# Kernel optimization log

Measured on AMD Instinct MI355X. Metric: run time of the kernel, lower is better.

The kernel has to match this reference:

```python
import jax, jax.numpy as jnp
import numpy as np

B, D, H, O, E, K = 8192, 1024, 4096, 1024, 8, 2

def setup_inputs() -> dict:
    key = jax.random.key(0)
    ks = jax.random.split(key, 8)
    x = jax.random.normal(ks[0], (B, D), dtype=jnp.float32)
    topk_idx = jax.random.randint(ks[1], (B, K), 0, E, dtype=jnp.int32)
    weights = jax.random.uniform(ks[2], (B, K), dtype=jnp.float32)
    s1 = 1.0 / np.sqrt(D)
    s2 = 1.0 / np.sqrt(H)
    W1 = jax.random.uniform(ks[3], (E, D, H), minval=-s1, maxval=s1, dtype=jnp.float32)
    b1 = jax.random.uniform(ks[4], (E, H), minval=-s1, maxval=s1, dtype=jnp.float32)
    W2 = jax.random.uniform(ks[5], (E, H, O), minval=-s2, maxval=s2, dtype=jnp.float32)
    b2 = jax.random.uniform(ks[6], (E, O), minval=-s2, maxval=s2, dtype=jnp.float32)
    return {"x": x, "topk_idx": topk_idx, "weights": weights,
            "W1": W1, "b1": b1, "W2": W2, "b2": b2}

def reference(x, topk_idx, weights, W1, b1, W2, b2):
    # Per-token gate mass for each expert: gate[b,e] = sum_i weights[b,i]*[topk_idx[b,i]==e]
    # Equivalent to the original masked gather/scatter combine (duplicates in topk_idx sum).
    out = jnp.zeros((x.shape[0], W2.shape[-1]), dtype=x.dtype)
    for e in range(W1.shape[0]):  # small fixed loop over experts
        gate_e = jnp.sum(weights * (topk_idx == e), axis=1)  # [B]
        h = jax.nn.relu(x @ W1[e] + b1[e])                   # [B,H]
        out_e = h @ W2[e] + b2[e]                            # [B,O]
        out = out + gate_e[:, None] * out_e
    return out
```

## Files before the change

### kernel.cpp

```cpp
#include <hip/hip_runtime.h>
#include <stdint.h>

#define B_TOK 8192
#define D_DIM 1024
#define H_DIM 4096
#define O_DIM 1024
#define E_NUM 8
#define K_TOP 2
#define NPAIR (B_TOK * K_TOP)

typedef short bf16x8 __attribute__((ext_vector_type(8)));
typedef float f32x4 __attribute__((ext_vector_type(4)));

struct Hdr {
    int counts[8];
    int offsets[9];
    int cursor[8];
    int total1, total2;
    int base1[9];
    int base2[9];
};

__device__ __forceinline__ unsigned short f2bf(float f) {
    union { float f; unsigned int u; } v; v.f = f;
    unsigned int u = v.u;
    unsigned int r = (u + 0x7fffu + ((u >> 16) & 1u)) >> 16;
    return (unsigned short)r;
}

__device__ __forceinline__ float bf2f(unsigned short s) {
    union { unsigned int u; float f; } v;
    v.u = ((unsigned int)s) << 16;
    return v.f;
}

__device__ __forceinline__ void async16(const void* g, const void* l) {
    __builtin_amdgcn_global_load_lds(
        (__attribute__((address_space(1))) void*)(uintptr_t)g,
        (__attribute__((address_space(3))) void*)(uint32_t)(uintptr_t)l,
        16, 0, 0);
}


__global__ void cvt_x_kernel(const float* __restrict__ x, unsigned short* __restrict__ xb) {
    int i = (blockIdx.x * 256 + threadIdx.x) * 4;
    float4 v = *(const float4*)(x + i);
    ushort4 o;
    o.x = f2bf(v.x); o.y = f2bf(v.y); o.z = f2bf(v.z); o.w = f2bf(v.w);
    *(ushort4*)(xb + i) = o;
}

__global__ __launch_bounds__(256) void tconv_kernel(const float* __restrict__ in,
                                                    unsigned short* __restrict__ out,
                                                    int R, int C) {
    __shared__ float t[64 * 69];
    int e = blockIdx.z;
    const float* ip = in + (size_t)e * R * C;
    unsigned short* op = out + (size_t)e * R * C;
    int c0 = blockIdx.x * 64, r0 = blockIdx.y * 64;
    int tid = threadIdx.x;
    int lr = tid >> 4;
    int lc = (tid & 15) * 4;
#pragma unroll
    for (int i = 0; i < 4; i++) {
        int row = lr + i * 16;
        float4 v = *(const float4*)&ip[(size_t)(r0 + row) * C + c0 + lc];
        t[row * 69 + lc + 0] = v.x;
        t[row * 69 + lc + 1] = v.y;
        t[row * 69 + lc + 2] = v.z;
        t[row * 69 + lc + 3] = v.w;
    }
    __syncthreads();
#pragma unroll
    for (int i = 0; i < 4; i++) {
        int c = lr + i * 16;
        ushort4 o;
        o.x = f2bf(t[(lc + 0) * 69 + c]);
        o.y = f2bf(t[(lc + 1) * 69 + c]);
        o.z = f2bf(t[(lc + 2) * 69 + c]);
        o.w = f2bf(t[(lc + 3) * 69 + c]);
        *(ushort4*)&op[(size_t)(c0 + c) * R + r0 + lc] = o;
    }
}


__global__ void route_count_kernel(const int* __restrict__ topk, Hdr* hdr) {
    __shared__ int cnt[8];
    int tid = threadIdx.x;
    if (tid < 8) cnt[tid] = 0;
    __syncthreads();
    for (int i = tid; i < NPAIR; i += 1024) atomicAdd(&cnt[topk[i]], 1);
    __syncthreads();
    if (tid == 0) {
        int off = 0, t1 = 0, t2 = 0;
        for (int e = 0; e < 8; e++) {
            int c = cnt[e];
            hdr->counts[e] = c;
            hdr->offsets[e] = off;
            hdr->cursor[e] = off;
            hdr->base1[e] = t1;
            hdr->base2[e] = t2;
            int mt = (c + 255) >> 8;
            t1 += mt * (H_DIM / 256);
            t2 += mt * (O_DIM / 256);
            off += c;
        }
        hdr->offsets[8] = off;
        hdr->base1[8] = t1;
        hdr->base2[8] = t2;
        hdr->total1 = t1;
        hdr->total2 = t2;
    }
}

__global__ void route_fill_kernel(const int* __restrict__ topk, const float* __restrict__ wts,
                                  Hdr* hdr, int* __restrict__ ptok, float* __restrict__ pgate,
                                  int* __restrict__ pslot) {
    int i = blockIdx.x * 256 + threadIdx.x;
    int e = topk[i];
    int pos = atomicAdd(&hdr->cursor[e], 1);
    ptok[pos] = i >> 1;
    pgate[pos] = wts[i];
    pslot[i] = pos;
}

__global__ void ws_fail_kernel(float* out) { out[0] = 1.0e9f; }


#define ASL(BUF, KH) ((BUF) * 32768 + (KH) * 16384)

#define STG_A(BUF, KH, KOFF) do { \
    async16(Ab + srcA[0] + (KOFF), smem + ASL(BUF, KH) + wu * 2048); \
    async16(Ab + srcA[1] + (KOFF), smem + ASL(BUF, KH) + wu * 2048 + 1024); } while (0)

#define STG_B(BUF, KH, KOFF) do { \
    async16(Bb + srcB[0] + (KOFF), smem + 65536 + ASL(BUF, KH) + wu * 2048); \
    async16(Bb + srcB[1] + (KOFF), smem + 65536 + ASL(BUF, KH) + wu * 2048 + 1024); } while (0)

#define VM6 asm volatile("s_waitcnt vmcnt(6)" ::: "memory")
#define VM0 asm volatile("s_waitcnt vmcnt(0)" ::: "memory")
#define NOPX ((void)0)

#define PHASE0(BUF, KH, STAGE, CKPT) do { \
    STAGE; \
    bq[0] = *(const bf16x8*)&smem[pBo[0] + ASL(BUF, KH)]; \
    bq[1] = *(const bf16x8*)&smem[pBo[1] + ASL(BUF, KH)]; \
    bq[2] = *(const bf16x8*)&smem[pBo[2] + ASL(BUF, KH)]; \
    bq[3] = *(const bf16x8*)&smem[pBo[3] + ASL(BUF, KH)]; \
    aq[0] = *(const bf16x8*)&smem[pAo[0] + ASL(BUF, KH)]; \
    aq[1] = *(const bf16x8*)&smem[pAo[1] + ASL(BUF, KH)]; \
    aq[2] = *(const bf16x8*)&smem[pAo[2] + ASL(BUF, KH)]; \
    aq[3] = *(const bf16x8*)&smem[pAo[3] + ASL(BUF, KH)]; \
    __builtin_amdgcn_s_barrier(); \
    asm volatile("s_waitcnt lgkmcnt(0)" ::: "memory"); \
    __builtin_amdgcn_s_setprio(1); \
    _Pragma("unroll") \
    for (int q_ = 0; q_ < 4; ++q_) { \
        _Pragma("unroll") \
        for (int n_ = 0; n_ < 4; ++n_) \
            acc[q_][n_] = __builtin_amdgcn_mfma_f32_16x16x32_bf16(aq[q_], bq[n_], acc[q_][n_], 0, 0, 0); \
    } \
    __builtin_amdgcn_s_setprio(0); \
    CKPT; \
    __builtin_amdgcn_s_barrier(); \
} while (0)

#define PHASE1(BUF, KH, STAGE, CKPT) do { \
    STAGE; \
    aq[0] = *(const bf16x8*)&smem[pAo[4] + ASL(BUF, KH)]; \
    aq[1] = *(const bf16x8*)&smem[pAo[5] + ASL(BUF, KH)]; \
    aq[2] = *(const bf16x8*)&smem[pAo[6] + ASL(BUF, KH)]; \
    aq[3] = *(const bf16x8*)&smem[pAo[7] + ASL(BUF, KH)]; \
    __builtin_amdgcn_s_barrier(); \
    asm volatile("s_waitcnt lgkmcnt(0)" ::: "memory"); \
    __builtin_amdgcn_s_setprio(1); \
    _Pragma("unroll") \
    for (int q_ = 0; q_ < 4; ++q_) { \
        _Pragma("unroll") \
        for (int n_ = 0; n_ < 4; ++n_) \
            acc[4 + q_][n_] = __builtin_amdgcn_mfma_f32_16x16x32_bf16(aq[q_], bq[n_], acc[4 + q_][n_], 0, 0, 0); \
    } \
    __builtin_amdgcn_s_setprio(0); \
    CKPT; \
    __builtin_amdgcn_s_barrier(); \
} while (0)

template <int KD, int N, bool GATHER>
__global__ __launch_bounds__(512, 2) void moe_gemm_kernel(
    const unsigned short* __restrict__ A,
    const unsigned short* __restrict__ Bt,
    const float* __restrict__ bias,
    const Hdr* __restrict__ hdr,
    const int* __restrict__ ptok,
    unsigned short* __restrict__ outp) {

    extern __shared__ __align__(16) char smem[];
    constexpr int NT = KD / 64;
    constexpr int NI = NT / 2;
    static_assert(NT >= 4 && (NT % 2) == 0, "K-tile count");

    const int tid = threadIdx.x;
    const int lane = tid & 63;
    const int wv = tid >> 6;
    const int wu = __builtin_amdgcn_readfirstlane(wv);
    const int lr = lane & 15;
    const int lkg = lane >> 4;
    const int wr = wv >> 2;
    const int wc = wv & 3;

    const int total = GATHER ? hdr->total1 : hdr->total2;
    const int* tb = GATHER ? hdr->base1 : hdr->base2;

    int chunk = (total + 7) >> 3;
    int seq = (blockIdx.x & 7) * chunk + (blockIdx.x >> 3);
    if (seq >= total) return;

    int e = 0;
#pragma unroll
    for (int j = 1; j < 8; j++)
        if (seq >= tb[j]) e = j;
    e = __builtin_amdgcn_readfirstlane(e);
    int lt = seq - tb[e];
    int cnt = hdr->counts[e], off = hdr->offsets[e];
    int MT = (cnt + 255) >> 8;
    int mtile = lt % MT, ntile = lt / MT;
    int m0 = mtile * 256, n0 = ntile * 256;

    const char* Ab = (const char*)A;
    const char* Bb = (const char*)(Bt + (size_t)e * ((size_t)N * KD));

    uint32_t srcA[2], srcB[2];
#pragma unroll
    for (int l = 0; l < 2; ++l) {
        int p = wv * 128 + l * 64 + lane;
        int rp = p >> 2, cp = p & 3;
        int r = rp ^ ((rp >> 2) & 1);
        int c = cp ^ (r & 3);
        int q = off + m0 + r;
        q = q > NPAIR - 1 ? NPAIR - 1 : q;
        uint32_t rowA = GATHER ? (uint32_t)ptok[q] : (uint32_t)q;
        srcA[l] = rowA * (uint32_t)(KD * 2) + (uint32_t)(c * 16);
        srcB[l] = (uint32_t)(n0 + r) * (uint32_t)(KD * 2) + (uint32_t)(c * 16);
    }

    uint32_t pAo[8], pBo[4];
#pragma unroll
    for (int mr = 0; mr < 8; ++mr) {
        int r = wr * 128 + mr * 16 + lr;
        pAo[mr] = (uint32_t)((r ^ ((r >> 2) & 1)) * 64 + (lkg ^ (r & 3)) * 16);
    }
#pragma unroll
    for (int nr = 0; nr < 4; ++nr) {
        int r = wc * 64 + nr * 16 + lr;
        pBo[nr] = (uint32_t)(65536 + (r ^ ((r >> 2) & 1)) * 64 + (lkg ^ (r & 3)) * 16);
    }

    f32x4 acc[8][4];
#pragma unroll
    for (int i = 0; i < 8; ++i)
#pragma unroll
        for (int j = 0; j < 4; ++j)
            acc[i][j] = (f32x4){0.f, 0.f, 0.f, 0.f};
    bf16x8 aq[4], bq[4];

    STG_A(0, 0, 0u);   STG_B(0, 0, 0u);
    STG_A(0, 1, 64u);  STG_B(0, 1, 64u);
    STG_A(1, 0, 128u); STG_B(1, 0, 128u);
    STG_B(1, 1, 192u);
    VM0;
    __builtin_amdgcn_s_barrier();

    for (int it = 0; it < NI - 1; ++it) {
        const uint32_t kb = (uint32_t)it * 256u;
        PHASE0(0, 0, STG_A(1, 1, kb + 192u), NOPX);
        PHASE1(0, 0, STG_B(0, 0, kb + 256u), NOPX);
        PHASE0(0, 1, STG_A(0, 0, kb + 256u), NOPX);
        PHASE1(0, 1, STG_B(0, 1, kb + 320u), VM6);
        PHASE0(1, 0, STG_A(0, 1, kb + 320u), NOPX);
        PHASE1(1, 0, STG_B(1, 0, kb + 384u), NOPX);
        PHASE0(1, 1, STG_A(1, 0, kb + 384u), NOPX);
        PHASE1(1, 1, STG_B(1, 1, kb + 448u), VM6);
    }
    {
        const uint32_t kb = (uint32_t)(NI - 1) * 256u;
        PHASE0(0, 0, STG_A(1, 1, kb + 192u), NOPX);
        PHASE1(0, 0, NOPX, NOPX);
        PHASE0(0, 1, NOPX, NOPX);
        PHASE1(0, 1, NOPX, VM0);
        PHASE0(1, 0, NOPX, NOPX);
        PHASE1(1, 0, NOPX, NOPX);
        PHASE0(1, 1, NOPX, NOPX);
        PHASE1(1, 1, NOPX, NOPX);
    }

    int rows_valid = cnt - m0;
    if (rows_valid > 256) rows_valid = 256;
#pragma unroll
    for (int nr = 0; nr < 4; ++nr) {
        int n = wc * 64 + nr * 16 + lr;
        float bv = bias[(size_t)e * N + n0 + n];
#pragma unroll
        for (int mr = 0; mr < 8; ++mr) {
#pragma unroll
            for (int r2 = 0; r2 < 4; ++r2) {
                int m = wr * 128 + mr * 16 + lkg * 4 + r2;
                float v = acc[mr][nr][r2] + bv;
                if (GATHER) v = v > 0.f ? v : 0.f;
                *(unsigned short*)&smem[(m * 256 + n) * 2] = f2bf(v);
            }
        }
    }
    __syncthreads();
#pragma unroll
    for (int j = 0; j < 16; ++j) {
        int idx = j * 512 + tid;
        int row = idx >> 5;
        int c16 = idx & 31;
        if (row < rows_valid) {
            uint4 v = *(const uint4*)&smem[row * 512 + c16 * 16];
            *(uint4*)&outp[(size_t)(off + m0 + row) * N + n0 + c16 * 8] = v;
        }
    }
}

__global__ void combine_kernel(const unsigned short* __restrict__ oslot,
                               const int* __restrict__ pslot,
                               const float* __restrict__ wts,
                               float* __restrict__ out) {
    int tok = blockIdx.x;
    int s0 = pslot[tok * 2], s1 = pslot[tok * 2 + 1];
    float g0 = wts[tok * 2], g1 = wts[tok * 2 + 1];
    int n = threadIdx.x * 4;
    ushort4 a = *(const ushort4*)&oslot[(size_t)s0 * O_DIM + n];
    ushort4 b = *(const ushort4*)&oslot[(size_t)s1 * O_DIM + n];
    float4 o;
    o.x = g0 * bf2f(a.x) + g1 * bf2f(b.x);
    o.y = g0 * bf2f(a.y) + g1 * bf2f(b.y);
    o.z = g0 * bf2f(a.z) + g1 * bf2f(b.z);
    o.w = g0 * bf2f(a.w) + g1 * bf2f(b.w);
    *(float4*)&out[(size_t)tok * O_DIM + n] = o;
}


extern "C" void kernel_launch(void* const* d_in, const int* in_sizes, int n_in,
                              void* d_out, int out_size, void* d_ws, size_t ws_size,
                              hipStream_t stream) {
    const float* x   = (const float*)d_in[0];
    const int* topk  = (const int*)d_in[1];
    const float* wts = (const float*)d_in[2];
    const float* W1  = (const float*)d_in[3];
    const float* b1  = (const float*)d_in[4];
    const float* W2  = (const float*)d_in[5];
    const float* b2  = (const float*)d_in[6];
    float* out = (float*)d_out;

    char* ws = (char*)d_ws;
    size_t off = 0;
    auto alloc = [&](size_t bytes) -> void* {
        void* p = ws + off;
        off += (bytes + 255) & ~(size_t)255;
        return p;
    };
    Hdr* hdr = (Hdr*)alloc(sizeof(Hdr));
    int* ptok = (int*)alloc((size_t)NPAIR * 4);
    float* pgate = (float*)alloc((size_t)NPAIR * 4);
    int* pslot = (int*)alloc((size_t)NPAIR * 4);
    unsigned short* xb   = (unsigned short*)alloc((size_t)B_TOK * D_DIM * 2);
    unsigned short* W1bt = (unsigned short*)alloc((size_t)E_NUM * D_DIM * H_DIM * 2);
    unsigned short* W2bt = (unsigned short*)alloc((size_t)E_NUM * H_DIM * O_DIM * 2);
    unsigned short* hbuf = (unsigned short*)alloc((size_t)NPAIR * H_DIM * 2);
    unsigned short* oslot = W1bt;

    if (off > ws_size) {
        hipMemsetAsync(d_out, 0, (size_t)out_size * sizeof(float), stream);
        ws_fail_kernel<<<1, 1, 0, stream>>>(out);
        return;
    }

    static int attr_done = 0;
    if (!attr_done) {
        (void)hipFuncSetAttribute(
            reinterpret_cast<const void*>(&moe_gemm_kernel<D_DIM, H_DIM, true>),
            hipFuncAttributeMaxDynamicSharedMemorySize, 131072);
        (void)hipFuncSetAttribute(
            reinterpret_cast<const void*>(&moe_gemm_kernel<H_DIM, O_DIM, false>),
            hipFuncAttributeMaxDynamicSharedMemorySize, 131072);
        attr_done = 1;
    }

    cvt_x_kernel<<<(B_TOK * D_DIM) / 1024, 256, 0, stream>>>(x, xb);
    tconv_kernel<<<dim3(H_DIM / 64, D_DIM / 64, E_NUM), dim3(256), 0, stream>>>(W1, W1bt, D_DIM, H_DIM);
    tconv_kernel<<<dim3(O_DIM / 64, H_DIM / 64, E_NUM), dim3(256), 0, stream>>>(W2, W2bt, H_DIM, O_DIM);
    route_count_kernel<<<1, 1024, 0, stream>>>(topk, hdr);
    route_fill_kernel<<<NPAIR / 256, 256, 0, stream>>>(topk, wts, hdr, ptok, pgate, pslot);

    moe_gemm_kernel<D_DIM, H_DIM, true><<<1152, 512, 131072, stream>>>(
        xb, W1bt, b1, hdr, ptok, hbuf);
    moe_gemm_kernel<H_DIM, O_DIM, false><<<288, 512, 131072, stream>>>(
        hbuf, W2bt, b2, hdr, ptok, oslot);
    combine_kernel<<<B_TOK, 256, 0, stream>>>(oslot, pslot, wts, out);
}
```

Measured before the change: 802.8 us.

## Use 128x128 tiled kernel for second MoE GEMM and change LDS swizzle

The down-projection GEMM now runs on a new 128x128-tile kernel with grouped tile ordering and 1152 blocks instead of the 256x256 pipelined kernel with 288 blocks, so more CUs are occupied. The routing header counts second-GEMM tiles at 128-row granularity. The first GEMM swaps its XOR LDS swizzle for an additive rotation and writes the epilogue in two padded passes to reduce bank conflicts. The new kernel has no software pipelining (load, sync, compute), which may cost throughput per tile.

```diff
diff --git a/kernel.cpp b/kernel.cpp
--- a/kernel.cpp
+++ b/kernel.cpp
@@ -100,9 +100,10 @@
             hdr->cursor[e] = off;
             hdr->base1[e] = t1;
             hdr->base2[e] = t2;
-            int mt = (c + 255) >> 8;
-            t1 += mt * (H_DIM / 256);
-            t2 += mt * (O_DIM / 256);
+            int mt1 = (c + 255) >> 8;
+            int mt2 = (c + 127) >> 7;
+            t1 += mt1 * (H_DIM / 256);
+            t2 += mt2 * (O_DIM / 128);
             off += c;
         }
         hdr->offsets[8] = off;
@@ -186,7 +187,7 @@
 } while (0)
 
 template <int KD, int N, bool GATHER>
-__global__ __launch_bounds__(512, 2) void moe_gemm_kernel(
+__global__ __launch_bounds__(512, 2) void moe_gemm256_kernel(
     const unsigned short* __restrict__ A,
     const unsigned short* __restrict__ Bt,
     const float* __restrict__ bias,
@@ -208,8 +209,8 @@
     const int wr = wv >> 2;
     const int wc = wv & 3;
 
-    const int total = GATHER ? hdr->total1 : hdr->total2;
-    const int* tb = GATHER ? hdr->base1 : hdr->base2;
+    const int total = hdr->total1;
+    const int* tb = hdr->base1;
 
     int chunk = (total + 7) >> 3;
     int seq = (blockIdx.x & 7) * chunk + (blockIdx.x >> 3);
@@ -232,27 +233,26 @@
     uint32_t srcA[2], srcB[2];
 #pragma unroll
     for (int l = 0; l < 2; ++l) {
-        int p = wv * 128 + l * 64 + lane;
-        int rp = p >> 2, cp = p & 3;
-        int r = rp ^ ((rp >> 2) & 1);
-        int c = cp ^ (r & 3);
-        int q = off + m0 + r;
+        int g = wv * 128 + l * 64 + lane;
+        int rp = g >> 2, cp = g & 3;
+        int c = (cp - (rp >> 1)) & 3;
+        int q = off + m0 + rp;
         q = q > NPAIR - 1 ? NPAIR - 1 : q;
         uint32_t rowA = GATHER ? (uint32_t)ptok[q] : (uint32_t)q;
         srcA[l] = rowA * (uint32_t)(KD * 2) + (uint32_t)(c * 16);
-        srcB[l] = (uint32_t)(n0 + r) * (uint32_t)(KD * 2) + (uint32_t)(c * 16);
+        srcB[l] = (uint32_t)(n0 + rp) * (uint32_t)(KD * 2) + (uint32_t)(c * 16);
     }
 
     uint32_t pAo[8], pBo[4];
 #pragma unroll
     for (int mr = 0; mr < 8; ++mr) {
         int r = wr * 128 + mr * 16 + lr;
-        pAo[mr] = (uint32_t)((r ^ ((r >> 2) & 1)) * 64 + (lkg ^ (r & 3)) * 16);
+        pAo[mr] = (uint32_t)(r * 64 + ((lkg + (r >> 1)) & 3) * 16);
     }
 #pragma unroll
     for (int nr = 0; nr < 4; ++nr) {
         int r = wc * 64 + nr * 16 + lr;
-        pBo[nr] = (uint32_t)(65536 + (r ^ ((r >> 2) & 1)) * 64 + (lkg ^ (r & 3)) * 16);
+        pBo[nr] = (uint32_t)(65536 + r * 64 + ((lkg + (r >> 1)) & 3) * 16);
     }
 
     f32x4 acc[8][4];
@@ -293,32 +293,177 @@
         PHASE1(1, 1, NOPX, NOPX);
     }
 
+    unsigned short* eb = (unsigned short*)smem;
     int rows_valid = cnt - m0;
     if (rows_valid > 256) rows_valid = 256;
 #pragma unroll
-    for (int nr = 0; nr < 4; ++nr) {
-        int n = wc * 64 + nr * 16 + lr;
+    for (int pass = 0; pass < 2; ++pass) {
+        __syncthreads();
+        if (wr == pass) {
+#pragma unroll
+            for (int nr = 0; nr < 4; ++nr) {
+                int n = wc * 64 + nr * 16 + lr;
+                float bv = bias[(size_t)e * N + n0 + n];
+#pragma unroll
+                for (int mr = 0; mr < 8; ++mr) {
+#pragma unroll
+                    for (int r2 = 0; r2 < 4; ++r2) {
+                        int ml = mr * 16 + lkg * 4 + r2;
+                        float v = acc[mr][nr][r2] + bv;
+                        if (GATHER) v = v > 0.f ? v : 0.f;
+                        eb[ml * 264 + n] = f2bf(v);
+                    }
+                }
+            }
+        }
+        __syncthreads();
+        int rv = rows_valid - pass * 128;
+        if (rv > 128) rv = 128;
+#pragma unroll
+        for (int j = 0; j < 8; ++j) {
+            int idx = j * 512 + tid;
+            int row = idx >> 5;
+            int c16 = idx & 31;
+            if (row < rv) {
+                uint4 v = *(const uint4*)&eb[row * 264 + c16 * 8];
+                *(uint4*)&outp[(size_t)(off + m0 + pass * 128 + row) * N + n0 + c16 * 8] = v;
+            }
+        }
+    }
+}
+
+template <int K, int N, bool GATHER>
+__global__ __launch_bounds__(256, 4) void moe_gemm128_kernel(
+    const unsigned short* __restrict__ A,
+    const unsigned short* __restrict__ Bt,
+    const float* __restrict__ bias,
+    const Hdr* __restrict__ hdr,
+    const int* __restrict__ ptok,
+    unsigned short* __restrict__ outp) {
+
+    __shared__ __align__(16) unsigned short smem[128 * 132];
+    unsigned short* As = smem;
+    unsigned short* Bs = smem + 128 * 64;
+
+    const int tid = threadIdx.x;
+    const int lane = tid & 63;
+    const int wv = tid >> 6;
+    const int wu = __builtin_amdgcn_readfirstlane(wv);
+    const int wm = (wv & 1) * 64;
+    const int wn = (wv >> 1) * 64;
+    const int lr = lane & 15;
+    const int lkg = lane >> 4;
+
+    const int total = hdr->total2;
+    const int* tb = hdr->base2;
+    constexpr int NT = N / 128;
+
+    int chunk = (total + 7) >> 3;
+    int seq = (blockIdx.x & 7) * chunk + (blockIdx.x >> 3);
+    if (seq >= total) return;
+
+    int e = 0;
+#pragma unroll
+    for (int j = 1; j < 8; j++)
+        if (seq >= tb[j]) e = j;
+    e = __builtin_amdgcn_readfirstlane(e);
+    int lt = seq - tb[e];
+    int cnt = hdr->counts[e], off = hdr->offsets[e];
+    int MT = (cnt + 127) >> 7;
+
+    int band = lt / (NT * 8);
+    int r = lt - band * (NT * 8);
+    int mrem = MT - band * 8;
+    mrem = mrem > 8 ? 8 : mrem;
+    int gsz = mrem * 8;
+    int g = r / gsz;
+    int rg = r - g * gsz;
+    int gm = rg % mrem;
+    int gn = rg / mrem;
+    int mtile = band * 8 + gm;
+    int ntile = g * 8 + gn;
+    int m0 = mtile * 128, n0 = ntile * 128;
+
+    const char* Ab = (const char*)A;
+    const char* Bb = (const char*)(Bt + (size_t)e * ((size_t)N * K));
+    uint32_t offA[4], offB[4];
+#pragma unroll
+    for (int i = 0; i < 4; i++) {
+        int s = i * 256 + tid;
+        int rr = s >> 3;
+        int cl = (s & 7) ^ (rr & 7);
+        int p = off + m0 + rr;
+        p = p > NPAIR - 1 ? NPAIR - 1 : p;
+        uint32_t row = GATHER ? (uint32_t)ptok[p] : (uint32_t)p;
+        offA[i] = (row * (uint32_t)K + (uint32_t)cl * 8u) * 2u;
+        offB[i] = (((uint32_t)(n0 + rr)) * (uint32_t)K + (uint32_t)cl * 8u) * 2u;
+    }
+
+    f32x4 zero = {0.f, 0.f, 0.f, 0.f};
+    f32x4 acc[4][4];
+#pragma unroll
+    for (int mt = 0; mt < 4; mt++)
+#pragma unroll
+        for (int nt = 0; nt < 4; nt++) acc[mt][nt] = zero;
+
+    for (int k0 = 0; k0 < K; k0 += 64) {
+#pragma unroll
+        for (int i = 0; i < 4; i++) {
+            async16(Ab + offA[i], &As[(i * 256 + wu * 64) * 8]);
+            async16(Bb + offB[i], &Bs[(i * 256 + wu * 64) * 8]);
+            offA[i] += 128;
+            offB[i] += 128;
+        }
+        __syncthreads();
+#pragma unroll
+        for (int ks = 0; ks < 2; ks++) {
+            bf16x8 af[4];
+#pragma unroll
+            for (int q = 0; q < 4; q++) {
+                int ra = wm + q * 16 + lr;
+                int ca = (ks * 4 + lkg) ^ (ra & 7);
+                af[q] = *(const bf16x8*)&As[ra * 64 + ca * 8];
+            }
+#pragma unroll
+            for (int nt = 0; nt < 4; nt++) {
+                int rb = wn + nt * 16 + lr;
+                int cb = (ks * 4 + lkg) ^ (rb & 7);
+                bf16x8 bfr = *(const bf16x8*)&Bs[rb * 64 + cb * 8];
+#pragma unroll
+                for (int mt = 0; mt < 4; mt++)
+                    acc[mt][nt] = __builtin_amdgcn_mfma_f32_16x16x32_bf16(
+                        af[mt], bfr, acc[mt][nt], 0, 0, 0);
+            }
+        }
+        __syncthreads();
+    }
+
+#pragma unroll
+    for (int nt = 0; nt < 4; nt++) {
+        int n = wn + nt * 16 + lr;
         float bv = bias[(size_t)e * N + n0 + n];
 #pragma unroll
-        for (int mr = 0; mr < 8; ++mr) {
-#pragma unroll
-            for (int r2 = 0; r2 < 4; ++r2) {
-                int m = wr * 128 + mr * 16 + lkg * 4 + r2;
-                float v = acc[mr][nr][r2] + bv;
+        for (int mt = 0; mt < 4; mt++) {
+#pragma unroll
+            for (int r2 = 0; r2 < 4; r2++) {
+                int m = wm + mt * 16 + lkg * 4 + r2;
+                float v = acc[mt][nt][r2] + bv;
                 if (GATHER) v = v > 0.f ? v : 0.f;
-                *(unsigned short*)&smem[(m * 256 + n) * 2] = f2bf(v);
+                smem[m * 132 + n] = f2bf(v);
             }
         }
     }
     __syncthreads();
-#pragma unroll
-    for (int j = 0; j < 16; ++j) {
-        int idx = j * 512 + tid;
+    int rows_valid = cnt - m0;
+    if (rows_valid > 128) rows_valid = 128;
+#pragma unroll
+    for (int j = 0; j < 16; j++) {
+        int idx = j * 256 + tid;
         int row = idx >> 5;
-        int c16 = idx & 31;
+        int lc8 = idx & 31;
         if (row < rows_valid) {
-            uint4 v = *(const uint4*)&smem[row * 512 + c16 * 16];
-            *(uint4*)&outp[(size_t)(off + m0 + row) * N + n0 + c16 * 8] = v;
+            uint2 v = *(const uint2*)&smem[row * 132 + lc8 * 4];
+            *(uint2*)&outp[(size_t)(off + m0 + row) * N + n0 + lc8 * 4] = v;
         }
     }
 }
@@ -380,10 +525,7 @@
     static int attr_done = 0;
     if (!attr_done) {
         (void)hipFuncSetAttribute(
-            reinterpret_cast<const void*>(&moe_gemm_kernel<D_DIM, H_DIM, true>),
-            hipFuncAttributeMaxDynamicSharedMemorySize, 131072);
-        (void)hipFuncSetAttribute(
-            reinterpret_cast<const void*>(&moe_gemm_kernel<H_DIM, O_DIM, false>),
+            reinterpret_cast<const void*>(&moe_gemm256_kernel<D_DIM, H_DIM, true>),
             hipFuncAttributeMaxDynamicSharedMemorySize, 131072);
         attr_done = 1;
     }
@@ -394,9 +536,9 @@
     route_count_kernel<<<1, 1024, 0, stream>>>(topk, hdr);
     route_fill_kernel<<<NPAIR / 256, 256, 0, stream>>>(topk, wts, hdr, ptok, pgate, pslot);
 
-    moe_gemm_kernel<D_DIM, H_DIM, true><<<1152, 512, 131072, stream>>>(
+    moe_gemm256_kernel<D_DIM, H_DIM, true><<<1152, 512, 131072, stream>>>(
         xb, W1bt, b1, hdr, ptok, hbuf);
-    moe_gemm_kernel<H_DIM, O_DIM, false><<<288, 512, 131072, stream>>>(
+    moe_gemm128_kernel<H_DIM, O_DIM, false><<<1152, 256, 0, stream>>>(
         hbuf, W2bt, b2, hdr, ptok, oslot);
     combine_kernel<<<B_TOK, 256, 0, stream>>>(oslot, pslot, wts, out);
 }
```

After: 769.1 us. -4.2%, faster.
